# Kernel optimization log

Hardware: AMD Instinct MI355X
Metric: run time of the kernel (lower is better)

The kernel has to match this reference:

```python
import jax, jax.numpy as jnp
import numpy as np

EPS = 1e-5          # nn.LayerNorm default eps
THRESH = 0.4        # min_entity_score
K = 20              # max_entities_per_text
NUM_TYPES = 8       # len(EntityType) (not in source; fixed constant)


def _mlp(x, w1, b1, g, be, w2, b2):
    """Linear -> LayerNorm -> GELU(exact) -> (Dropout=eval identity) -> Linear."""
    h = x @ w1 + b1
    mu = h.mean(-1, keepdims=True)
    var = ((h - mu) ** 2).mean(-1, keepdims=True)
    h = (h - mu) * jax.lax.rsqrt(var + EPS) * g + be
    h = jax.nn.gelu(h, approximate=False)
    return h @ w2 + b2


def setup_inputs() -> dict:
    key = jax.random.key(0)
    ks = jax.random.split(key, 10)
    B, S, D, H, T = 8, 4096, 1024, 256, NUM_TYPES

    def lin(k, i, o):
        s = 1.0 / np.sqrt(i)
        return jax.random.uniform(k, (i, o), jnp.float32, -s, s)

    return {
        "hidden_states": jax.random.normal(ks[0], (B, S, D), jnp.float32),
        "attention_mask": jax.random.randint(ks[1], (B, S), 0, 2).astype(jnp.int32),
        # entity_scorer params
        "sc_w1": lin(ks[2], D, H), "sc_b1": jnp.zeros((H,), jnp.float32),
        "sc_g": jnp.ones((H,), jnp.float32), "sc_be": jnp.zeros((H,), jnp.float32),
        "sc_w2": lin(ks[3], H, 1), "sc_b2": jnp.zeros((1,), jnp.float32),
        # span_enhancer params
        "en_w1": lin(ks[4], D, H), "en_b1": jnp.zeros((H,), jnp.float32),
        "en_g": jnp.ones((H,), jnp.float32), "en_be": jnp.zeros((H,), jnp.float32),
        "en_w2": lin(ks[5], H, D), "en_b2": jnp.zeros((D,), jnp.float32),
        # type_classifier params
        "ty_w1": lin(ks[6], D, H), "ty_b1": jnp.zeros((H,), jnp.float32),
        "ty_g": jnp.ones((H,), jnp.float32), "ty_be": jnp.zeros((H,), jnp.float32),
        "ty_w2": lin(ks[7], H, T), "ty_b2": jnp.zeros((T,), jnp.float32),
    }


def reference(hidden_states, attention_mask,
              sc_w1, sc_b1, sc_g, sc_be, sc_w2, sc_b2,
              en_w1, en_b1, en_g, en_be, en_w2, en_b2,
              ty_w1, ty_b1, ty_g, ty_be, ty_w2, ty_b2):
    B, S, D = hidden_states.shape
    # per-token entity scores [B, S]
    scores = jax.nn.sigmoid(_mlp(hidden_states, sc_w1, sc_b1, sc_g, sc_be, sc_w2, sc_b2))[..., 0]
    scores = scores * attention_mask.astype(scores.dtype)
    # parallel run-length encoding of spans (replaces serial python loop):
    # a token is inside a span iff score >= thresh and unmasked; spans break on
    # below-threshold or masked tokens, exactly as the serial RLE does.
    above = (scores >= THRESH) & (attention_mask > 0)
    prev = jnp.pad(above[:, :-1], ((0, 0), (1, 0)))
    start = above & ~prev
    sid = jnp.clip(jnp.cumsum(start.astype(jnp.int32), axis=1) - 1, 0)  # span label per token
    seg = (sid + jnp.arange(B, dtype=jnp.int32)[:, None] * S).reshape(-1)
    w = above.astype(scores.dtype)
    nseg = B * S
    span_len = jax.ops.segment_sum(w.reshape(-1), seg, num_segments=nseg).reshape(B, S)
    span_sum = jax.ops.segment_sum((scores * w).reshape(-1), seg, num_segments=nseg).reshape(B, S)
    rep_sum = jax.ops.segment_sum((hidden_states * w[..., None]).reshape(B * S, D), seg,
                                  num_segments=nseg).reshape(B, S, D)
    denom = jnp.maximum(span_len, 1.0)
    avg = span_sum / denom                      # mean token score per span
    valid = (span_len > 0) & (avg >= THRESH)    # avg-score threshold from original
    sel = jnp.where(valid, avg, -1.0)
    # keep at most K highest-scoring spans per batch row (matches global sort + per-batch cap)
    top_vals, top_idx = jax.lax.top_k(sel, K)   # [B, K]
    valid_k = (top_vals >= THRESH).astype(scores.dtype)
    reps = jnp.take_along_axis(rep_sum, top_idx[..., None], axis=1)
    lens = jnp.take_along_axis(denom, top_idx, axis=1)
    reps = reps / lens[..., None] * valid_k[..., None]      # span mean-pooled hidden states
    enhanced = _mlp(reps, en_w1, en_b1, en_g, en_be, en_w2, en_b2) * valid_k[..., None]
    type_logits = _mlp(enhanced, ty_w1, ty_b1, ty_g, ty_be, ty_w2, ty_b2)
    type_probs = jax.nn.softmax(type_logits, axis=-1)
    entity_types = jnp.argmax(type_logits, axis=-1)
    entity_scores = top_vals * valid_k
    return scores, enhanced, type_logits, entity_scores, type_probs, entity_types, valid_k
```

## Files before the change

### kernel.cpp

```cpp
#include <hip/hip_runtime.h>
#include <hip/hip_bf16.h>

#define S_LEN 4096
#define BATCH 8
#define DMODEL 1024
#define HDIM 256
#define NTYPES 8
#define KMAX 20
#define NSLOT (BATCH*KMAX)
#define THRESH 0.4f
#define LN_EPS 1e-5f
#define RSQRT2 0.70710678118654752f

#define O_SCORES 0
#define O_ENH    32768
#define O_TLOG   196608
#define O_ESC    197888
#define O_TPROB  198048
#define O_TYPE   199328
#define O_VALIDK 199488

#define WS_SCORES   0
#define WS_SPSTART  32768
#define WS_SPLEN    49152
#define WS_SPAVG    65536
#define WS_NSP      81920
#define WS_SELSTART 81936
#define WS_SELLEN   82096
#define WS_SELAVG   82256
#define WS_SELVALID 82416
#define WS_IMG      82576

typedef _Float16 f16x8 __attribute__((ext_vector_type(8)));
typedef float f32x16 __attribute__((ext_vector_type(16)));

__device__ __forceinline__ float gelu_exact(float v) {
    return 0.5f * v * (1.0f + erff(v * RSQRT2));
}
__device__ __forceinline__ int kkey(int r) { return (r ^ (r >> 2)) & 3; }

#define GLL16(g, l) __builtin_amdgcn_global_load_lds( \
    (const __attribute__((address_space(1))) unsigned int*)(g), \
    (__attribute__((address_space(3))) unsigned int*)(l), 16, 0, 0)

__global__ __launch_bounds__(256) void k_prep(
    const float* __restrict__ W1, _Float16* __restrict__ IMG)
{
    const int c = blockIdx.x;
    const int n = threadIdx.x;
#pragma unroll
    for (int j = 0; j < 4; j++) {
        f16x8 hv, lv;
#pragma unroll
        for (int e = 0; e < 8; e++) {
            float w = W1[(size_t)(c * 32 + j * 8 + e) * HDIM + n];
            _Float16 h = (_Float16)w;
            hv[e] = h;
            lv[e] = (_Float16)(w - (float)h);
        }
        int off = c * 16384 + n * 32 + ((j ^ kkey(n)) * 8);
        *(f16x8*)&IMG[off] = hv;
        *(f16x8*)&IMG[off + 8192] = lv;
    }
}

__global__ __launch_bounds__(512, 2) void k_score4(
    const float* __restrict__ X, const _Float16* __restrict__ IMG,
    const float* __restrict__ B1, const float* __restrict__ G,
    const float* __restrict__ BE, const float* __restrict__ W2,
    const float* __restrict__ B2, const int* __restrict__ MASK,
    float* __restrict__ scf, float* __restrict__ out)
{
    union SM {
        struct {
            _Float16 A[2][2][4096];
            _Float16 B[3][16384];
        } s;
        struct { float part2[128 * 3]; float mul[128]; float rsl[128]; } e;
    };
    __shared__ SM sm;

    const int tid = threadIdx.x;
    const int lane = tid & 63, wid = tid >> 6;
    const int lr = lane & 31, lh = lane >> 5;
    const int wm = (wid & 3) * 32;
    const int wn = (wid >> 2) * 128;
    const int wg = wid >> 2;
    const int tok0 = blockIdx.x * 128;

    const int arow = tid >> 2, akg = tid & 3;
    const int aoff = arow * 32 + ((akg ^ kkey(arow)) * 8);
    const float* xptr = X + (size_t)(tok0 + arow) * DMODEL + akg * 8;
    const char* gB = (const char*)IMG + wid * 4096 + lane * 16;

    f32x16 acc[4];
#pragma unroll
    for (int ni = 0; ni < 4; ni++) acc[ni] = (f32x16)0.0f;

    {
        float4 xa = *(const float4*)xptr;
        float4 xb = *(const float4*)(xptr + 4);
        char* lB0 = (char*)sm.s.B[0] + wid * 4096;
        char* lB1 = (char*)sm.s.B[1] + wid * 4096;
#pragma unroll
        for (int r = 0; r < 4; r++) GLL16(gB + r * 1024, lB0 + r * 1024);
#pragma unroll
        for (int r = 0; r < 4; r++) GLL16(gB + 32768 + r * 1024, lB1 + r * 1024);
        float xv[8] = {xa.x, xa.y, xa.z, xa.w, xb.x, xb.y, xb.z, xb.w};
        f16x8 ah, al;
#pragma unroll
        for (int e = 0; e < 8; e++) {
            _Float16 h = (_Float16)xv[e];
            ah[e] = h;
            al[e] = (_Float16)(xv[e] - (float)h);
        }
        *(f16x8*)&sm.s.A[0][0][aoff] = ah;
        *(f16x8*)&sm.s.A[0][1][aoff] = al;
    }
    asm volatile("s_waitcnt vmcnt(4) lgkmcnt(0)" ::: "memory");
    __builtin_amdgcn_s_barrier();
    __builtin_amdgcn_sched_barrier(0);

    int bc = 0;
    int ac = 0;
    for (int c = 0; c < 32; ++c) {
        const int cn = (c + 1) & 31;
        const int c2 = (c + 2) & 31;
        int b2 = bc - 1; if (b2 < 0) b2 = 2;
        float4 nxa = *(const float4*)(xptr + cn * 32);
        float4 nxb = *(const float4*)(xptr + cn * 32 + 4);
        {
            char* lB = (char*)sm.s.B[b2] + wid * 4096;
            const char* g = (const char*)IMG + (size_t)c2 * 32768 + wid * 4096 + lane * 16;
#pragma unroll
            for (int r = 0; r < 4; r++) GLL16(g + r * 1024, lB + r * 1024);
        }
        {
            const _Float16* Ah = sm.s.A[ac][0];
            const _Float16* Al = sm.s.A[ac][1];
            const _Float16* Bc = sm.s.B[bc];
#pragma unroll
            for (int s = 0; s < 2; ++s) {
                const int kg = s * 2 + lh;
                const int row = wm + lr;
                const int oa = row * 32 + ((kg ^ kkey(row)) * 8);
                f16x8 fah = *(const f16x8*)&Ah[oa];
                f16x8 fal = *(const f16x8*)&Al[oa];
#pragma unroll
                for (int ni = 0; ni < 4; ni++) {
                    const int col = wn + ni * 32 + lr;
                    const int ob = col * 32 + ((kg ^ kkey(col)) * 8);
                    f16x8 fbh = *(const f16x8*)&Bc[ob];
                    f16x8 fbl = *(const f16x8*)&Bc[8192 + ob];
                    acc[ni] = __builtin_amdgcn_mfma_f32_32x32x16_f16(fah, fbh, acc[ni], 0, 0, 0);
                    acc[ni] = __builtin_amdgcn_mfma_f32_32x32x16_f16(fal, fbh, acc[ni], 0, 0, 0);
                    acc[ni] = __builtin_amdgcn_mfma_f32_32x32x16_f16(fah, fbl, acc[ni], 0, 0, 0);
                }
            }
        }
        {
            float xv[8] = {nxa.x, nxa.y, nxa.z, nxa.w, nxb.x, nxb.y, nxb.z, nxb.w};
            f16x8 ah, al;
#pragma unroll
            for (int e = 0; e < 8; e++) {
                _Float16 h = (_Float16)xv[e];
                ah[e] = h;
                al[e] = (_Float16)(xv[e] - (float)h);
            }
            *(f16x8*)&sm.s.A[ac ^ 1][0][aoff] = ah;
            *(f16x8*)&sm.s.A[ac ^ 1][1][aoff] = al;
        }
        asm volatile("s_waitcnt vmcnt(4) lgkmcnt(0)" ::: "memory");
        __builtin_amdgcn_s_barrier();
        __builtin_amdgcn_sched_barrier(0);
        bc = bc == 2 ? 0 : bc + 1;
        ac ^= 1;
    }

    __syncthreads();

    float bcol[4], gcol[4], becol[4], wcol[4];
#pragma unroll
    for (int ni = 0; ni < 4; ni++) {
        int colg = wn + ni * 32 + lr;
        bcol[ni] = B1[colg];
        gcol[ni] = G[colg];
        becol[ni] = BE[colg];
        wcol[ni] = W2[colg];
    }
#pragma unroll
    for (int ni = 0; ni < 4; ni++)
#pragma unroll
        for (int r = 0; r < 16; r++) acc[ni][r] += bcol[ni];

#pragma unroll
    for (int r = 0; r < 16; r++) {
        float p = acc[0][r] + acc[1][r] + acc[2][r] + acc[3][r];
        p += __shfl_xor(p, 1);  p += __shfl_xor(p, 2);
        p += __shfl_xor(p, 4);  p += __shfl_xor(p, 8);
        p += __shfl_xor(p, 16);
        int row = wm + (r & 3) + 8 * (r >> 2) + 4 * lh;
        if (lr == 0) sm.e.part2[row * 3 + wg] = p;
    }
    __syncthreads();
    if (tid < 128)
        sm.e.mul[tid] = (sm.e.part2[tid * 3] + sm.e.part2[tid * 3 + 1]) * (1.0f / 256.0f);
    __syncthreads();
#pragma unroll
    for (int r = 0; r < 16; r++) {
        int row = wm + (r & 3) + 8 * (r >> 2) + 4 * lh;
        float m = sm.e.mul[row];
        float p = 0.0f;
#pragma unroll
        for (int ni = 0; ni < 4; ni++) {
            float d = acc[ni][r] - m;
            p += d * d;
        }
        p += __shfl_xor(p, 1);  p += __shfl_xor(p, 2);
        p += __shfl_xor(p, 4);  p += __shfl_xor(p, 8);
        p += __shfl_xor(p, 16);
        if (lr == 0) sm.e.part2[row * 3 + wg] = p;
    }
    __syncthreads();
    if (tid < 128)
        sm.e.rsl[tid] = rsqrtf((sm.e.part2[tid * 3] + sm.e.part2[tid * 3 + 1]) * (1.0f / 256.0f) + LN_EPS);
    __syncthreads();
#pragma unroll
    for (int r = 0; r < 16; r++) {
        int row = wm + (r & 3) + 8 * (r >> 2) + 4 * lh;
        float m = sm.e.mul[row];
        float rv = sm.e.rsl[row];
        float p = 0.0f;
#pragma unroll
        for (int ni = 0; ni < 4; ni++) {
            float v = (acc[ni][r] - m) * rv * gcol[ni] + becol[ni];
            p += gelu_exact(v) * wcol[ni];
        }
        p += __shfl_xor(p, 1);  p += __shfl_xor(p, 2);
        p += __shfl_xor(p, 4);  p += __shfl_xor(p, 8);
        p += __shfl_xor(p, 16);
        if (lr == 0) sm.e.part2[row * 3 + wg] = p;
    }
    __syncthreads();
    if (tid < 128) {
        float s = sm.e.part2[tid * 3] + sm.e.part2[tid * 3 + 1];
        float logit = s + B2[0];
        float sc = 1.0f / (1.0f + expf(-logit));
        int t = tok0 + tid;
        sc *= (float)MASK[t];
        scf[t] = sc;
        out[O_SCORES + t] = sc;
    }
}

__global__ __launch_bounds__(1024) void k_spans(
    const float* __restrict__ scf, int* __restrict__ spstart,
    int* __restrict__ splen, float* __restrict__ spavg, int* __restrict__ nsp,
    int* __restrict__ selstart, int* __restrict__ sellen,
    float* __restrict__ selavg, float* __restrict__ selvalid,
    float* __restrict__ out)
{
    const int r = blockIdx.x, tid = threadIdx.x;
    __shared__ float sc[S_LEN];
    __shared__ unsigned char ab[S_LEN];
    __shared__ int scn[1024];
    __shared__ float avgl[2048];
    __shared__ float rv[16];
    __shared__ int ri[16];

    float4 v = ((const float4*)(scf + (size_t)r * S_LEN))[tid];
    const int s0 = tid * 4;
    sc[s0 + 0] = v.x; sc[s0 + 1] = v.y; sc[s0 + 2] = v.z; sc[s0 + 3] = v.w;
    ab[s0 + 0] = (v.x >= THRESH);
    ab[s0 + 1] = (v.y >= THRESH);
    ab[s0 + 2] = (v.z >= THRESH);
    ab[s0 + 3] = (v.w >= THRESH);
    __syncthreads();

    bool st[4];
    int cnt = 0;
#pragma unroll
    for (int i = 0; i < 4; i++) {
        bool a = ab[s0 + i] != 0;
        bool p = (s0 + i == 0) ? false : (ab[s0 + i - 1] != 0);
        st[i] = a && !p;
        cnt += st[i] ? 1 : 0;
    }
    scn[tid] = cnt;
    __syncthreads();
    for (int off = 1; off < 1024; off <<= 1) {
        int mine = scn[tid];
        int add = (tid >= off) ? scn[tid - off] : 0;
        __syncthreads();
        scn[tid] = mine + add;
        __syncthreads();
    }
    const int total = scn[1023];
    int j = scn[tid] - cnt;
    for (int i = 0; i < 4; i++) {
        if (st[i]) {
            int s = s0 + i;
            float sum = 0.0f;
            int len = 0;
            int e = s;
            while (e < S_LEN && ab[e]) { sum += sc[e]; len++; e++; }
            float avg = sum / (float)len;
            spstart[r * 2048 + j] = s;
            splen[r * 2048 + j] = len;
            spavg[r * 2048 + j] = avg;
            avgl[j] = avg;
            j++;
        }
    }
    if (tid == 0) nsp[r] = total;
    __syncthreads();

    for (int k = 0; k < KMAX; k++) {
        float bv = -3.0e38f;
        int bi = 0x7FFFFFFF;
        for (int q = tid; q < total; q += 1024) {
            float a = avgl[q];
            if (a > bv) { bv = a; bi = q; }
        }
#pragma unroll
        for (int m = 1; m < 64; m <<= 1) {
            float ov = __shfl_xor(bv, m);
            int oi = __shfl_xor(bi, m);
            if (ov > bv || (ov == bv && oi < bi)) { bv = ov; bi = oi; }
        }
        if ((tid & 63) == 0) { rv[tid >> 6] = bv; ri[tid >> 6] = bi; }
        __syncthreads();
        if (tid < 64) {
            float v2 = (tid < 16) ? rv[tid] : -3.0e38f;
            int i2 = (tid < 16) ? ri[tid] : 0x7FFFFFFF;
#pragma unroll
            for (int m = 1; m < 16; m <<= 1) {
                float ov = __shfl_xor(v2, m);
                int oi = __shfl_xor(i2, m);
                if (ov > v2 || (ov == v2 && oi < i2)) { v2 = ov; i2 = oi; }
            }
            if (tid == 0) {
                int slot = r * KMAX + k;
                if (k < total) {
                    avgl[i2] = -3.0e38f;
                    int ln = splen[r * 2048 + i2];
                    float vd = (v2 >= THRESH && ln > 0) ? 1.0f : 0.0f;
                    selstart[slot] = spstart[r * 2048 + i2];
                    sellen[slot] = ln;
                    selavg[slot] = v2;
                    selvalid[slot] = vd;
                    out[O_ESC + slot] = v2 * vd;
                    out[O_VALIDK + slot] = vd;
                } else {
                    selstart[slot] = -1;
                    sellen[slot] = 0;
                    selavg[slot] = -1.0f;
                    selvalid[slot] = 0.0f;
                    out[O_ESC + slot] = 0.0f;
                    out[O_VALIDK + slot] = 0.0f;
                }
            }
        }
        __syncthreads();
    }
}

__global__ __launch_bounds__(1024) void k_tail2(
    const float* __restrict__ X, const int* __restrict__ selstart,
    const int* __restrict__ sellen, const float* __restrict__ selvalid,
    const float* __restrict__ en_w1, const float* __restrict__ en_b1,
    const float* __restrict__ en_g, const float* __restrict__ en_be,
    const float* __restrict__ en_w2, const float* __restrict__ en_b2,
    const float* __restrict__ ty_w1, const float* __restrict__ ty_b1,
    const float* __restrict__ ty_g, const float* __restrict__ ty_be,
    const float* __restrict__ ty_w2, const float* __restrict__ ty_b2,
    float* __restrict__ out)
{
    const int slot = blockIdx.x, tid = threadIdx.x;
    __shared__ float xr[DMODEL];
    __shared__ float ps[DMODEL];
    __shared__ float g1[HDIM];
    __shared__ float red[8];
    __shared__ float lgp[4 * NTYPES];
    __shared__ float lg[NTYPES];

    const int r = slot / KMAX;
    const int s0 = selstart[slot], ln = sellen[slot];
    const float vd = selvalid[slot];
    const int j = tid & 255, p = tid >> 8;

    {
        float a = 0.0f;
        if (s0 >= 0) {
            const float* base = X + ((size_t)r * S_LEN + s0) * DMODEL + tid;
#pragma unroll 4
            for (int t = 0; t < ln; t++) a += base[(size_t)t * DMODEL];
        }
        const float dn = (ln > 0) ? (float)ln : 1.0f;
        xr[tid] = a / dn * vd;
    }
    __syncthreads();

    {
        float acc = 0.0f;
        const float* wp = en_w1 + (size_t)(p * 256) * HDIM + j;
        const float* xp = xr + p * 256;
#pragma unroll 16
        for (int k = 0; k < 256; k++) acc += xp[k] * wp[(size_t)k * HDIM];
        ps[tid] = acc;
    }
    __syncthreads();
    float h = 0.0f, mu = 0.0f;
    if (tid < 256) {
        h = ps[tid] + ps[256 + tid] + ps[512 + tid] + ps[768 + tid] + en_b1[tid];
        float s = h;
#pragma unroll
        for (int m = 1; m < 64; m <<= 1) s += __shfl_xor(s, m);
        if ((tid & 63) == 0) red[tid >> 6] = s;
    }
    __syncthreads();
    if (tid < 256) {
        mu = (red[0] + red[1] + red[2] + red[3]) * (1.0f / 256.0f);
        float d = h - mu;
        float s = d * d;
#pragma unroll
        for (int m = 1; m < 64; m <<= 1) s += __shfl_xor(s, m);
        if ((tid & 63) == 0) red[4 + (tid >> 6)] = s;
    }
    __syncthreads();
    if (tid < 256) {
        float var = (red[4] + red[5] + red[6] + red[7]) * (1.0f / 256.0f);
        float v = (h - mu) * rsqrtf(var + LN_EPS) * en_g[tid] + en_be[tid];
        g1[tid] = gelu_exact(v);
    }
    __syncthreads();

    {
        float acc = en_b2[tid];
        const float* wp = en_w2 + tid;
#pragma unroll 16
        for (int k = 0; k < 256; k++) acc += g1[k] * wp[(size_t)k * DMODEL];
        acc *= vd;
        out[O_ENH + (size_t)slot * DMODEL + tid] = acc;
        xr[tid] = acc;
    }
    __syncthreads();

    {
        float acc = 0.0f;
        const float* wp = ty_w1 + (size_t)(p * 256) * HDIM + j;
        const float* xp = xr + p * 256;
#pragma unroll 16
        for (int k = 0; k < 256; k++) acc += xp[k] * wp[(size_t)k * HDIM];
        ps[tid] = acc;
    }
    __syncthreads();
    h = 0.0f; mu = 0.0f;
    if (tid < 256) {
        h = ps[tid] + ps[256 + tid] + ps[512 + tid] + ps[768 + tid] + ty_b1[tid];
        float s = h;
#pragma unroll
        for (int m = 1; m < 64; m <<= 1) s += __shfl_xor(s, m);
        if ((tid & 63) == 0) red[tid >> 6] = s;
    }
    __syncthreads();
    if (tid < 256) {
        mu = (red[0] + red[1] + red[2] + red[3]) * (1.0f / 256.0f);
        float d = h - mu;
        float s = d * d;
#pragma unroll
        for (int m = 1; m < 64; m <<= 1) s += __shfl_xor(s, m);
        if ((tid & 63) == 0) red[4 + (tid >> 6)] = s;
    }
    __syncthreads();
    if (tid < 256) {
        float var = (red[4] + red[5] + red[6] + red[7]) * (1.0f / 256.0f);
        float v = (h - mu) * rsqrtf(var + LN_EPS) * ty_g[tid] + ty_be[tid];
        g1[tid] = gelu_exact(v);
    }
    __syncthreads();

    if (tid < 256) {
        float gv = g1[tid];
        float4 w0 = *(const float4*)&ty_w2[tid * NTYPES];
        float4 w1v = *(const float4*)&ty_w2[tid * NTYPES + 4];
        float pj[8] = {gv * w0.x, gv * w0.y, gv * w0.z, gv * w0.w,
                       gv * w1v.x, gv * w1v.y, gv * w1v.z, gv * w1v.w};
#pragma unroll
        for (int q = 0; q < 8; q++) {
            float s = pj[q];
#pragma unroll
            for (int m = 1; m < 64; m <<= 1) s += __shfl_xor(s, m);
            pj[q] = s;
        }
        if ((tid & 63) == 0) {
#pragma unroll
            for (int q = 0; q < 8; q++) lgp[(tid >> 6) * NTYPES + q] = pj[q];
        }
    }
    __syncthreads();
    if (tid < NTYPES) {
        float la = ty_b2[tid] + lgp[tid] + lgp[NTYPES + tid] +
                   lgp[2 * NTYPES + tid] + lgp[3 * NTYPES + tid];
        lg[tid] = la;
        out[O_TLOG + slot * NTYPES + tid] = la;
    }
    __syncthreads();
    if (tid == 0) {
        float mx = lg[0];
        int am = 0;
        for (int t = 1; t < NTYPES; t++)
            if (lg[t] > mx) { mx = lg[t]; am = t; }
        float ex[NTYPES], ssum = 0.0f;
        for (int t = 0; t < NTYPES; t++) { ex[t] = expf(lg[t] - mx); ssum += ex[t]; }
        for (int t = 0; t < NTYPES; t++)
            out[O_TPROB + slot * NTYPES + t] = ex[t] / ssum;
        out[O_TYPE + slot] = (float)am;
    }
}

extern "C" void kernel_launch(void* const* d_in, const int* in_sizes, int n_in,
                              void* d_out, int out_size, void* d_ws, size_t ws_size,
                              hipStream_t stream) {
    const float* X = (const float*)d_in[0];
    const int* MASK = (const int*)d_in[1];
    const float* sc_w1 = (const float*)d_in[2];
    const float* sc_b1 = (const float*)d_in[3];
    const float* sc_g  = (const float*)d_in[4];
    const float* sc_be = (const float*)d_in[5];
    const float* sc_w2 = (const float*)d_in[6];
    const float* sc_b2 = (const float*)d_in[7];
    const float* en_w1 = (const float*)d_in[8];
    const float* en_b1 = (const float*)d_in[9];
    const float* en_g  = (const float*)d_in[10];
    const float* en_be = (const float*)d_in[11];
    const float* en_w2 = (const float*)d_in[12];
    const float* en_b2 = (const float*)d_in[13];
    const float* ty_w1 = (const float*)d_in[14];
    const float* ty_b1 = (const float*)d_in[15];
    const float* ty_g  = (const float*)d_in[16];
    const float* ty_be = (const float*)d_in[17];
    const float* ty_w2 = (const float*)d_in[18];
    const float* ty_b2 = (const float*)d_in[19];

    float* out = (float*)d_out;
    float* wsf = (float*)d_ws;
    int* wsi = (int*)d_ws;
    _Float16* img = (_Float16*)(wsf + WS_IMG);

    k_prep<<<32, 256, 0, stream>>>(sc_w1, img);
    k_score4<<<(BATCH * S_LEN) / 128, 512, 0, stream>>>(
        X, img, sc_b1, sc_g, sc_be, sc_w2, sc_b2, MASK, wsf + WS_SCORES, out);
    k_spans<<<BATCH, 1024, 0, stream>>>(
        wsf + WS_SCORES, wsi + WS_SPSTART, wsi + WS_SPLEN, wsf + WS_SPAVG,
        wsi + WS_NSP, wsi + WS_SELSTART, wsi + WS_SELLEN, wsf + WS_SELAVG,
        wsf + WS_SELVALID, out);
    k_tail2<<<NSLOT, 1024, 0, stream>>>(
        X, wsi + WS_SELSTART, wsi + WS_SELLEN, wsf + WS_SELVALID,
        en_w1, en_b1, en_g, en_be, en_w2, en_b2,
        ty_w1, ty_b1, ty_g, ty_be, ty_w2, ty_b2, out);
}
```

Baseline: 154.6 us.

## Retile score GEMM warps to 64x64 and split k-chunk into barrier-separated MFMA phases

Changes the per-wave tile in the scoring GEMM from 32x128 to 64x64, so each wave loads two A and two B fragments instead of one A and four B, which lowers LDS read traffic per MFMA. The inner k-loop is split into two phases: fragments are loaded, then a block barrier and raised priority around the MFMA cluster, with the next B-chunk prefetch moved between the phases. The LayerNorm epilogue reductions are adapted to four column groups. The extra barriers per chunk add synchronisation cost, and the effect on overlap depends on how waves interleave.

```diff
diff --git a/kernel.cpp b/kernel.cpp
--- a/kernel.cpp
+++ b/kernel.cpp
@@ -64,7 +64,7 @@
     }
 }
 
-__global__ __launch_bounds__(512, 2) void k_score4(
+__global__ __launch_bounds__(512, 2) void k_score5(
     const float* __restrict__ X, const _Float16* __restrict__ IMG,
     const float* __restrict__ B1, const float* __restrict__ G,
     const float* __restrict__ BE, const float* __restrict__ W2,
@@ -76,16 +76,16 @@
             _Float16 A[2][2][4096];
             _Float16 B[3][16384];
         } s;
-        struct { float part2[128 * 3]; float mul[128]; float rsl[128]; } e;
+        struct { float part2[128 * 5]; float mul[128]; float rsl[128]; } e;
     };
     __shared__ SM sm;
 
     const int tid = threadIdx.x;
     const int lane = tid & 63, wid = tid >> 6;
     const int lr = lane & 31, lh = lane >> 5;
-    const int wm = (wid & 3) * 32;
-    const int wn = (wid >> 2) * 128;
-    const int wg = wid >> 2;
+    const int wm = (wid >> 2) * 64;
+    const int wn = (wid & 3) * 64;
+    const int wnid = wid & 3;
     const int tok0 = blockIdx.x * 128;
 
     const int arow = tid >> 2, akg = tid & 3;
@@ -93,9 +93,11 @@
     const float* xptr = X + (size_t)(tok0 + arow) * DMODEL + akg * 8;
     const char* gB = (const char*)IMG + wid * 4096 + lane * 16;
 
-    f32x16 acc[4];
-#pragma unroll
-    for (int ni = 0; ni < 4; ni++) acc[ni] = (f32x16)0.0f;
+    f32x16 acc[2][2];
+#pragma unroll
+    for (int mi = 0; mi < 2; mi++)
+#pragma unroll
+        for (int ni = 0; ni < 2; ni++) acc[mi][ni] = (f32x16)0.0f;
 
     {
         float4 xa = *(const float4*)xptr;
@@ -118,46 +120,96 @@
         *(f16x8*)&sm.s.A[0][1][aoff] = al;
     }
     asm volatile("s_waitcnt vmcnt(4) lgkmcnt(0)" ::: "memory");
+    __builtin_amdgcn_sched_barrier(0);
     __builtin_amdgcn_s_barrier();
-    __builtin_amdgcn_sched_barrier(0);
-
-    int bc = 0;
-    int ac = 0;
+
+    int bc = 0, ac = 0;
     for (int c = 0; c < 32; ++c) {
         const int cn = (c + 1) & 31;
         const int c2 = (c + 2) & 31;
         int b2 = bc - 1; if (b2 < 0) b2 = 2;
+        const _Float16* Ah = sm.s.A[ac][0];
+        const _Float16* Al = sm.s.A[ac][1];
+        const _Float16* Bc = sm.s.B[bc];
+
+        f16x8 fah0[2], fal0[2], fbh0[2], fbl0[2];
+        {
+            const int kg = lh;
+#pragma unroll
+            for (int mi = 0; mi < 2; mi++) {
+                int row = wm + mi * 32 + lr;
+                int oa = row * 32 + ((kg ^ kkey(row)) * 8);
+                fah0[mi] = *(const f16x8*)&Ah[oa];
+                fal0[mi] = *(const f16x8*)&Al[oa];
+            }
+#pragma unroll
+            for (int ni = 0; ni < 2; ni++) {
+                int col = wn + ni * 32 + lr;
+                int ob = col * 32 + ((kg ^ kkey(col)) * 8);
+                fbh0[ni] = *(const f16x8*)&Bc[ob];
+                fbl0[ni] = *(const f16x8*)&Bc[8192 + ob];
+            }
+        }
         float4 nxa = *(const float4*)(xptr + cn * 32);
         float4 nxb = *(const float4*)(xptr + cn * 32 + 4);
+        __builtin_amdgcn_sched_barrier(0);
+        __builtin_amdgcn_s_barrier();
+        asm volatile("s_waitcnt lgkmcnt(0)" ::: "memory");
+        __builtin_amdgcn_sched_barrier(0);
+        __builtin_amdgcn_s_setprio(1);
+#pragma unroll
+        for (int ni = 0; ni < 2; ni++)
+#pragma unroll
+            for (int mi = 0; mi < 2; mi++) {
+                acc[mi][ni] = __builtin_amdgcn_mfma_f32_32x32x16_f16(fah0[mi], fbh0[ni], acc[mi][ni], 0, 0, 0);
+                acc[mi][ni] = __builtin_amdgcn_mfma_f32_32x32x16_f16(fal0[mi], fbh0[ni], acc[mi][ni], 0, 0, 0);
+                acc[mi][ni] = __builtin_amdgcn_mfma_f32_32x32x16_f16(fah0[mi], fbl0[ni], acc[mi][ni], 0, 0, 0);
+            }
+        __builtin_amdgcn_s_setprio(0);
+        __builtin_amdgcn_sched_barrier(0);
+        __builtin_amdgcn_s_barrier();
+
+        f16x8 fah1[2], fal1[2], fbh1[2], fbl1[2];
+        {
+            const int kg = 2 + lh;
+#pragma unroll
+            for (int mi = 0; mi < 2; mi++) {
+                int row = wm + mi * 32 + lr;
+                int oa = row * 32 + ((kg ^ kkey(row)) * 8);
+                fah1[mi] = *(const f16x8*)&Ah[oa];
+                fal1[mi] = *(const f16x8*)&Al[oa];
+            }
+#pragma unroll
+            for (int ni = 0; ni < 2; ni++) {
+                int col = wn + ni * 32 + lr;
+                int ob = col * 32 + ((kg ^ kkey(col)) * 8);
+                fbh1[ni] = *(const f16x8*)&Bc[ob];
+                fbl1[ni] = *(const f16x8*)&Bc[8192 + ob];
+            }
+        }
         {
             char* lB = (char*)sm.s.B[b2] + wid * 4096;
             const char* g = (const char*)IMG + (size_t)c2 * 32768 + wid * 4096 + lane * 16;
 #pragma unroll
             for (int r = 0; r < 4; r++) GLL16(g + r * 1024, lB + r * 1024);
         }
-        {
-            const _Float16* Ah = sm.s.A[ac][0];
-            const _Float16* Al = sm.s.A[ac][1];
-            const _Float16* Bc = sm.s.B[bc];
-#pragma unroll
-            for (int s = 0; s < 2; ++s) {
-                const int kg = s * 2 + lh;
-                const int row = wm + lr;
-                const int oa = row * 32 + ((kg ^ kkey(row)) * 8);
-                f16x8 fah = *(const f16x8*)&Ah[oa];
-                f16x8 fal = *(const f16x8*)&Al[oa];
-#pragma unroll
-                for (int ni = 0; ni < 4; ni++) {
-                    const int col = wn + ni * 32 + lr;
-                    const int ob = col * 32 + ((kg ^ kkey(col)) * 8);
-                    f16x8 fbh = *(const f16x8*)&Bc[ob];
-                    f16x8 fbl = *(const f16x8*)&Bc[8192 + ob];
-                    acc[ni] = __builtin_amdgcn_mfma_f32_32x32x16_f16(fah, fbh, acc[ni], 0, 0, 0);
-                    acc[ni] = __builtin_amdgcn_mfma_f32_32x32x16_f16(fal, fbh, acc[ni], 0, 0, 0);
-                    acc[ni] = __builtin_amdgcn_mfma_f32_32x32x16_f16(fah, fbl, acc[ni], 0, 0, 0);
-                }
-            }
-        }
+        __builtin_amdgcn_sched_barrier(0);
+        __builtin_amdgcn_s_barrier();
+        asm volatile("s_waitcnt lgkmcnt(0)" ::: "memory");
+        __builtin_amdgcn_sched_barrier(0);
+        __builtin_amdgcn_s_setprio(1);
+#pragma unroll
+        for (int ni = 0; ni < 2; ni++)
+#pragma unroll
+            for (int mi = 0; mi < 2; mi++) {
+                acc[mi][ni] = __builtin_amdgcn_mfma_f32_32x32x16_f16(fah1[mi], fbh1[ni], acc[mi][ni], 0, 0, 0);
+                acc[mi][ni] = __builtin_amdgcn_mfma_f32_32x32x16_f16(fal1[mi], fbh1[ni], acc[mi][ni], 0, 0, 0);
+                acc[mi][ni] = __builtin_amdgcn_mfma_f32_32x32x16_f16(fah1[mi], fbl1[ni], acc[mi][ni], 0, 0, 0);
+            }
+        __builtin_amdgcn_s_setprio(0);
+        __builtin_amdgcn_sched_barrier(0);
+        __builtin_amdgcn_s_barrier();
+
         {
             float xv[8] = {nxa.x, nxa.y, nxa.z, nxa.w, nxb.x, nxb.y, nxb.z, nxb.w};
             f16x8 ah, al;
@@ -171,17 +223,17 @@
             *(f16x8*)&sm.s.A[ac ^ 1][1][aoff] = al;
         }
         asm volatile("s_waitcnt vmcnt(4) lgkmcnt(0)" ::: "memory");
+        __builtin_amdgcn_sched_barrier(0);
         __builtin_amdgcn_s_barrier();
-        __builtin_amdgcn_sched_barrier(0);
         bc = bc == 2 ? 0 : bc + 1;
         ac ^= 1;
     }
 
     __syncthreads();
 
-    float bcol[4], gcol[4], becol[4], wcol[4];
-#pragma unroll
-    for (int ni = 0; ni < 4; ni++) {
+    float bcol[2], gcol[2], becol[2], wcol[2];
+#pragma unroll
+    for (int ni = 0; ni < 2; ni++) {
         int colg = wn + ni * 32 + lr;
         bcol[ni] = B1[colg];
         gcol[ni] = G[colg];
@@ -189,61 +241,68 @@
         wcol[ni] = W2[colg];
     }
 #pragma unroll
-    for (int ni = 0; ni < 4; ni++)
-#pragma unroll
-        for (int r = 0; r < 16; r++) acc[ni][r] += bcol[ni];
-
-#pragma unroll
-    for (int r = 0; r < 16; r++) {
-        float p = acc[0][r] + acc[1][r] + acc[2][r] + acc[3][r];
-        p += __shfl_xor(p, 1);  p += __shfl_xor(p, 2);
-        p += __shfl_xor(p, 4);  p += __shfl_xor(p, 8);
-        p += __shfl_xor(p, 16);
-        int row = wm + (r & 3) + 8 * (r >> 2) + 4 * lh;
-        if (lr == 0) sm.e.part2[row * 3 + wg] = p;
-    }
+    for (int mi = 0; mi < 2; mi++)
+#pragma unroll
+        for (int ni = 0; ni < 2; ni++)
+#pragma unroll
+            for (int r = 0; r < 16; r++) acc[mi][ni][r] += bcol[ni];
+
+#pragma unroll
+    for (int mi = 0; mi < 2; mi++)
+#pragma unroll
+        for (int r = 0; r < 16; r++) {
+            float p = acc[mi][0][r] + acc[mi][1][r];
+            p += __shfl_xor(p, 1);  p += __shfl_xor(p, 2);
+            p += __shfl_xor(p, 4);  p += __shfl_xor(p, 8);
+            p += __shfl_xor(p, 16);
+            int row = wm + mi * 32 + (r & 3) + 8 * (r >> 2) + 4 * lh;
+            if (lr == 0) sm.e.part2[row * 5 + wnid] = p;
+        }
     __syncthreads();
     if (tid < 128)
-        sm.e.mul[tid] = (sm.e.part2[tid * 3] + sm.e.part2[tid * 3 + 1]) * (1.0f / 256.0f);
-    __syncthreads();
-#pragma unroll
-    for (int r = 0; r < 16; r++) {
-        int row = wm + (r & 3) + 8 * (r >> 2) + 4 * lh;
-        float m = sm.e.mul[row];
-        float p = 0.0f;
-#pragma unroll
-        for (int ni = 0; ni < 4; ni++) {
-            float d = acc[ni][r] - m;
-            p += d * d;
-        }
-        p += __shfl_xor(p, 1);  p += __shfl_xor(p, 2);
-        p += __shfl_xor(p, 4);  p += __shfl_xor(p, 8);
-        p += __shfl_xor(p, 16);
-        if (lr == 0) sm.e.part2[row * 3 + wg] = p;
-    }
+        sm.e.mul[tid] = (sm.e.part2[tid * 5] + sm.e.part2[tid * 5 + 1] +
+                         sm.e.part2[tid * 5 + 2] + sm.e.part2[tid * 5 + 3]) * (1.0f / 256.0f);
+    __syncthreads();
+#pragma unroll
+    for (int mi = 0; mi < 2; mi++)
+#pragma unroll
+        for (int r = 0; r < 16; r++) {
+            int row = wm + mi * 32 + (r & 3) + 8 * (r >> 2) + 4 * lh;
+            float m = sm.e.mul[row];
+            float d0 = acc[mi][0][r] - m, d1 = acc[mi][1][r] - m;
+            float p = d0 * d0 + d1 * d1;
+            p += __shfl_xor(p, 1);  p += __shfl_xor(p, 2);
+            p += __shfl_xor(p, 4);  p += __shfl_xor(p, 8);
+            p += __shfl_xor(p, 16);
+            if (lr == 0) sm.e.part2[row * 5 + wnid] = p;
+        }
     __syncthreads();
     if (tid < 128)
-        sm.e.rsl[tid] = rsqrtf((sm.e.part2[tid * 3] + sm.e.part2[tid * 3 + 1]) * (1.0f / 256.0f) + LN_EPS);
-    __syncthreads();
-#pragma unroll
-    for (int r = 0; r < 16; r++) {
-        int row = wm + (r & 3) + 8 * (r >> 2) + 4 * lh;
-        float m = sm.e.mul[row];
-        float rv = sm.e.rsl[row];
-        float p = 0.0f;
-#pragma unroll
-        for (int ni = 0; ni < 4; ni++) {
-            float v = (acc[ni][r] - m) * rv * gcol[ni] + becol[ni];
-            p += gelu_exact(v) * wcol[ni];
-        }
-        p += __shfl_xor(p, 1);  p += __shfl_xor(p, 2);
-        p += __shfl_xor(p, 4);  p += __shfl_xor(p, 8);
-        p += __shfl_xor(p, 16);
-        if (lr == 0) sm.e.part2[row * 3 + wg] = p;
-    }
+        sm.e.rsl[tid] = rsqrtf((sm.e.part2[tid * 5] + sm.e.part2[tid * 5 + 1] +
+                                sm.e.part2[tid * 5 + 2] + sm.e.part2[tid * 5 + 3]) * (1.0f / 256.0f) + LN_EPS);
+    __syncthreads();
+#pragma unroll
+    for (int mi = 0; mi < 2; mi++)
+#pragma unroll
+        for (int r = 0; r < 16; r++) {
+            int row = wm + mi * 32 + (r & 3) + 8 * (r >> 2) + 4 * lh;
+            float m = sm.e.mul[row];
+            float rv = sm.e.rsl[row];
+            float p = 0.0f;
+#pragma unroll
+            for (int ni = 0; ni < 2; ni++) {
+                float v = (acc[mi][ni][r] - m) * rv * gcol[ni] + becol[ni];
+                p += gelu_exact(v) * wcol[ni];
+            }
+            p += __shfl_xor(p, 1);  p += __shfl_xor(p, 2);
+            p += __shfl_xor(p, 4);  p += __shfl_xor(p, 8);
+            p += __shfl_xor(p, 16);
+            if (lr == 0) sm.e.part2[row * 5 + wnid] = p;
+        }
     __syncthreads();
     if (tid < 128) {
-        float s = sm.e.part2[tid * 3] + sm.e.part2[tid * 3 + 1];
+        float s = sm.e.part2[tid * 5] + sm.e.part2[tid * 5 + 1] +
+                  sm.e.part2[tid * 5 + 2] + sm.e.part2[tid * 5 + 3];
         float logit = s + B2[0];
         float sc = 1.0f / (1.0f + expf(-logit));
         int t = tok0 + tid;
@@ -549,7 +608,7 @@
     _Float16* img = (_Float16*)(wsf + WS_IMG);
 
     k_prep<<<32, 256, 0, stream>>>(sc_w1, img);
-    k_score4<<<(BATCH * S_LEN) / 128, 512, 0, stream>>>(
+    k_score5<<<(BATCH * S_LEN) / 128, 512, 0, stream>>>(
         X, img, sc_b1, sc_g, sc_be, sc_w2, sc_b2, MASK, wsf + WS_SCORES, out);
     k_spans<<<BATCH, 1024, 0, stream>>>(
         wsf + WS_SCORES, wsi + WS_SPSTART, wsi + WS_SPLEN, wsf + WS_SPAVG,
```

After: 164.4 us. 1.06x slower.
